# Optimization experiments

Measured on AMD Instinct MI355X. Metric: run time of the kernel, lower is better.

## Reference

```python
import jax, jax.numpy as jnp
import numpy as np

N = 100000   # nodes
E = 3200000  # edges
G = 512      # graphs in batch
EPS = 1e-5   # batchnorm eps


def _lin(key, fan_in, fan_out):
    return jax.random.normal(key, (fan_in, fan_out), jnp.float32) / np.sqrt(fan_in)


def setup_inputs() -> dict:
    key = jax.random.key(0)
    ks = jax.random.split(key, 12)
    x = jax.random.normal(ks[0], (N, 2), jnp.float32)
    edge_index = jax.random.randint(ks[1], (2, E), 0, N, dtype=jnp.int64)
    batch_index = jnp.sort(jax.random.randint(ks[2], (N,), 0, G, dtype=jnp.int64))
    w = (8, 32, 128)
    return {
        "x": x, "edge_index": edge_index, "batch_index": batch_index,
        "W1": _lin(ks[3], 2, w[0]),   "b1": jnp.zeros((w[0],), jnp.float32),
        "g1": jnp.ones((w[0],), jnp.float32),  "be1": jnp.zeros((w[0],), jnp.float32),
        "W2": _lin(ks[4], w[0], w[1]), "b2": jnp.zeros((w[1],), jnp.float32),
        "g2": jnp.ones((w[1],), jnp.float32),  "be2": jnp.zeros((w[1],), jnp.float32),
        "W3": _lin(ks[5], w[1], w[2]), "b3": jnp.zeros((w[2],), jnp.float32),
        "g3": jnp.ones((w[2],), jnp.float32),  "be3": jnp.zeros((w[2],), jnp.float32),
        "Wl": _lin(ks[6], w[2], 3),    "bl": jnp.zeros((3,), jnp.float32),
    }


def _gcn_norm(edge_index):
    # add self loops, symmetric normalization (PyG GCNConv default)
    loops = jnp.arange(N, dtype=edge_index.dtype)
    src = jnp.concatenate([edge_index[0], loops])
    dst = jnp.concatenate([edge_index[1], loops])
    deg = jax.ops.segment_sum(jnp.ones_like(dst, jnp.float32), dst, num_segments=N)
    dis = jnp.where(deg > 0, jax.lax.rsqrt(jnp.maximum(deg, 1.0)), 0.0)
    norm = dis[src] * dis[dst]  # [E+N]
    return src, dst, norm


def _gcn_conv(h, W, b, src, dst, norm):
    h = h @ W                                   # [N, out]
    msg = h[src] * norm[:, None]                # gather + scale
    return jax.ops.segment_sum(msg, dst, num_segments=N) + b


def _bn(h, g, b):
    # training-mode batchnorm over node dim
    m = jnp.mean(h, axis=0)
    v = jnp.mean(jnp.square(h - m), axis=0)
    return (h - m) * jax.lax.rsqrt(v + EPS) * g + b


def reference(x, edge_index, batch_index, W1, b1, g1, be1, W2, b2, g2, be2,
              W3, b3, g3, be3, Wl, bl):
    src, dst, norm = _gcn_norm(edge_index)
    h = _bn(jax.nn.relu(_gcn_conv(x, W1, b1, src, dst, norm)), g1, be1)
    h = _bn(jax.nn.relu(_gcn_conv(h, W2, b2, src, dst, norm)), g2, be2)
    h = _bn(jax.nn.relu(_gcn_conv(h, W3, b3, src, dst, norm)), g3, be3)
    pooled = jax.ops.segment_max(h, batch_index, num_segments=G)  # [G, 128]
    logits = pooled @ Wl + bl                                     # [G, 3]
    return jax.nn.log_softmax(logits, axis=1)
```

## Files before the change

### kernel.cpp

```cpp
#include <hip/hip_runtime.h>
#include <hip/hip_bf16.h>
#include <hip/hip_fp16.h>
#include <math.h>

#define N_NODES 100000
#define N_EDGES 3200000
#define N_GRAPHS 512
#define BN_EPS 1e-5f
#define NBIN ((N_NODES + 511) / 512)
#define CHUNK 8192
#define NCHUNK ((N_EDGES + CHUNK - 1) / CHUNK)
#define STORE_CAP (N_EDGES + 16 * NBIN * NCHUNK)
#define LSEG 98
#define NSEGB ((N_NODES + LSEG - 1) / LSEG)
#define NSTATB ((N_NODES + 127) / 128)

typedef _Float16 half8_t __attribute__((ext_vector_type(8)));
typedef float float4_t __attribute__((ext_vector_type(4)));

struct alignas(8) h4 { __half2 a, b; };
struct alignas(16) h8s { __half2 h[4]; };


__global__ void k_hist2(const int* __restrict__ dst, int* __restrict__ hists) {
    __shared__ int h[NBIN];
    for (int i = threadIdx.x; i < NBIN; i += blockDim.x) h[i] = 0;
    __syncthreads();
    int e0 = blockIdx.x * CHUNK;
    int e1 = min(e0 + CHUNK, N_EDGES);
    for (int e = e0 + threadIdx.x; e < e1; e += blockDim.x)
        atomicAdd(&h[dst[e] >> 9], 1);
    __syncthreads();
    for (int i = threadIdx.x; i < NBIN; i += blockDim.x)
        hists[i * NCHUNK + blockIdx.x] = h[i];
}

__global__ void k_scan2(int* __restrict__ hists, int* __restrict__ ghist) {
    int b = blockIdx.x;
    int lane = threadIdx.x;
    int carry = 0;
    int base = b * NCHUNK;
    for (int c0 = 0; c0 < NCHUNK; c0 += 64) {
        int c = c0 + lane;
        int v = (c < NCHUNK) ? hists[base + c] : 0;
        int pv = (v + 15) & ~15;
        int inc = pv;
#pragma unroll
        for (int off = 1; off < 64; off <<= 1) {
            int u = __shfl_up(inc, off, 64);
            if (lane >= off) inc += u;
        }
        if (c < NCHUNK) hists[base + c] = inc - pv + carry;
        carry += __shfl(inc, 63, 64);
    }
    if (lane == 0) ghist[b] = carry;
}

__global__ void k_binscan(const int* __restrict__ ghist, int* __restrict__ bbase) {
    __shared__ int sd[512];
    int t = threadIdx.x;
    int v = (t < NBIN) ? ghist[t] : 0;
    sd[t] = v;
    __syncthreads();
    for (int off = 1; off < 512; off <<= 1) {
        int u = (t >= off) ? sd[t - off] : 0;
        __syncthreads();
        sd[t] += u;
        __syncthreads();
    }
    if (t < NBIN) bbase[t] = sd[t] - v;
    if (t == 511) bbase[NBIN] = sd[511];
}

__global__ void k_scatter(const int* __restrict__ src, const int* __restrict__ dst,
                          const int* __restrict__ bbase, const int* __restrict__ hists,
                          int* __restrict__ store) {
    __shared__ int cur[NBIN];
    for (int i = threadIdx.x; i < NBIN; i += blockDim.x)
        cur[i] = bbase[i] + hists[i * NCHUNK + blockIdx.x];
    __syncthreads();
    int e0 = blockIdx.x * CHUNK;
    int e1 = min(e0 + CHUNK, N_EDGES);
    for (int e = e0 + threadIdx.x; e < e1; e += blockDim.x) {
        int d = dst[e];
        int b = d >> 9;
        int pos = atomicAdd(&cur[b], 1);
        store[pos] = (src[e] << 9) | (d & 511);
    }
    __syncthreads();
    for (int i = threadIdx.x; i < NBIN; i += blockDim.x) {
        int p = cur[i];
        int end = (p + 15) & ~15;
        for (; p < end; ++p) store[p] = -1;
    }
}

__global__ void k_csr_build(const int* __restrict__ bbase, const int* __restrict__ store,
                            const float* __restrict__ x, int* __restrict__ offs,
                            int* __restrict__ ends, float* __restrict__ dis,
                            float* __restrict__ rdis, float4* __restrict__ xd,
                            int* __restrict__ csr) {
    __shared__ int cnt[512], cur[512], wsum[4];
    int b = blockIdx.x;
    int n0 = b << 9;
    int e0 = bbase[b], e1 = bbase[b + 1];
    int t = threadIdx.x;
    int lane = t & 63, wid = t >> 6;
    if (t < 512) cnt[t] = 0;
    __syncthreads();
    for (int e = e0 + t; e < e1; e += 1024) {
        int p = store[e];
        if (p >= 0) atomicAdd(&cnt[p & 511], 1);
    }
    __syncthreads();
    int c0 = 0, c1 = 0, pair = 0, inc = 0;
    if (t < 256) {
        c0 = cnt[2 * t];
        c1 = cnt[2 * t + 1];
        pair = c0 + c1;
        inc = pair;
#pragma unroll
        for (int off = 1; off < 64; off <<= 1) {
            int u = __shfl_up(inc, off, 64);
            if (lane >= off) inc += u;
        }
        if (lane == 63) wsum[wid] = inc;
    }
    __syncthreads();
    if (t < 256) {
        int wo = 0;
        for (int w = 0; w < wid; ++w) wo += wsum[w];
        int ex = inc - pair + wo;
        cur[2 * t] = ex;
        cur[2 * t + 1] = ex + c0;
#pragma unroll
        for (int j = 0; j < 2; ++j) {
            int n = n0 + 2 * t + j;
            int cc = j ? c1 : c0;
            int exx = j ? ex + c0 : ex;
            if (n < N_NODES) {
                offs[n] = e0 + exx;
                ends[n] = e0 + exx + cc;
                float dn = rsqrtf(1.0f + (float)cc);
                dis[n] = dn;
                rdis[n] = sqrtf(1.0f + (float)cc);
                float2 xv = *(const float2*)(x + 2 * (size_t)n);
                xd[n] = make_float4(dn * xv.x, dn * xv.y, dn, 0.f);
            } else if (n == N_NODES) {
                xd[N_NODES] = make_float4(0.f, 0.f, 0.f, 0.f);
            }
        }
    }
    __syncthreads();
    for (int e = e0 + t; e < e1; e += 1024) {
        int p = store[e];
        if (p >= 0) {
            int pos = e0 + atomicAdd(&cur[p & 511], 1);
            csr[pos] = p >> 9;
        }
    }
}


__global__ void k_agg1(const float4* __restrict__ xd, const int* __restrict__ offs,
                       const int* __restrict__ ends, const int* __restrict__ csr,
                       const float* __restrict__ W1, const float* __restrict__ b1,
                       float* __restrict__ svec, __half* __restrict__ ys1) {
    __shared__ float sW[16], sb[8];
    int t = threadIdx.x;
    if (t < 16) sW[t] = W1[t];
    if (t < 8) sb[t] = b1[t];
    __syncthreads();
    int wave = t >> 6, lane = t & 63;
    int nsub = lane >> 4, eg = lane & 15;
    int node = ((blockIdx.x * 4 + wave) << 2) + nsub;
    int e0 = offs[node], e1 = ends[node];
    float ax = 0.f, ay = 0.f, as = 0.f;
    for (int e = e0 + eg; e < e1; e += 32) {
        int s0 = csr[e];
        int s1 = (e + 16 < e1) ? csr[e + 16] : N_NODES;
        float4 v0 = xd[s0];
        float4 v1 = xd[s1];
        ax += v0.x + v1.x;
        ay += v0.y + v1.y;
        as += v0.z + v1.z;
    }
#pragma unroll
    for (int off = 1; off < 16; off <<= 1) {
        ax += __shfl_xor(ax, off, 64);
        ay += __shfl_xor(ay, off, 64);
        as += __shfl_xor(as, off, 64);
    }
    if (eg == 0) {
        float4 xn = xd[node];
        float dn = xn.z;
        float u0x = dn * (ax + xn.x);
        float u0y = dn * (ay + xn.y);
        svec[node] = dn * (as + xn.z);
        float y[8];
#pragma unroll
        for (int f = 0; f < 8; ++f)
            y[f] = dn * fmaxf(u0x * sW[f] + u0y * sW[8 + f] + sb[f], 0.f);
        h8s o;
#pragma unroll
        for (int q = 0; q < 4; ++q) o.h[q] = __floats2half2_rn(y[2 * q], y[2 * q + 1]);
        *(h8s*)(ys1 + (size_t)node * 8) = o;
    }
}


__global__ void k_prep2(const float* __restrict__ stats, const float* __restrict__ gamma,
                        const float* __restrict__ beta, const float* __restrict__ W2,
                        float* __restrict__ W2p, float* __restrict__ cw2,
                        __half* __restrict__ ys1) {
    __shared__ float a1[8], c1[8];
    int t = threadIdx.x;
    if (t < 8) {
        float inv_n = 1.0f / (float)N_NODES;
        float m = stats[t] * inv_n;
        float v = stats[8 + t] * inv_n - m * m;
        float a = gamma[t] * rsqrtf(v + BN_EPS);
        a1[t] = a;
        c1[t] = beta[t] - m * a;
    }
    __syncthreads();
    W2p[t] = a1[t >> 5] * W2[t];
    if (t < 32) {
        float cb = 0.f;
#pragma unroll
        for (int i = 0; i < 8; ++i) cb += c1[i] * W2[i * 32 + t];
        cw2[t] = cb;
    }
    if (t == 128) *(int4*)(ys1 + (size_t)N_NODES * 8) = make_int4(0, 0, 0, 0);
}


__global__ void k_agg2(const __half* __restrict__ ys1, const int* __restrict__ offs,
                       const int* __restrict__ ends, const int* __restrict__ csr,
                       const float* __restrict__ dis, const float* __restrict__ svec,
                       const float* __restrict__ W2p, const float* __restrict__ cw2,
                       const float* __restrict__ b2, __half* __restrict__ ys2) {
    __shared__ float sW[256], sC[32], sB[32];
    int t = threadIdx.x;
    sW[t] = W2p[t];
    if (t < 32) { sC[t] = cw2[t]; sB[t] = b2[t]; }
    __syncthreads();
    int wave = t >> 6, lane = t & 63;
    int nsub = lane >> 3, eg = (lane >> 1) & 3, chunk = lane & 1;
    int node = ((blockIdx.x * 4 + wave) << 3) + nsub;
    int e0 = offs[node], e1 = ends[node];
    float a0 = 0.f, a1 = 0.f, a2 = 0.f, a3 = 0.f;
    const __half* hp = ys1 + chunk * 4;
    for (int e = e0 + eg; e < e1; e += 8) {
        int s0 = csr[e];
        int s1 = (e + 4 < e1) ? csr[e + 4] : N_NODES;
        h4 v0 = *(const h4*)(hp + (size_t)s0 * 8);
        h4 v1 = *(const h4*)(hp + (size_t)s1 * 8);
        a0 += __low2float(v0.a) + __low2float(v1.a);
        a1 += __high2float(v0.a) + __high2float(v1.a);
        a2 += __low2float(v0.b) + __low2float(v1.b);
        a3 += __high2float(v0.b) + __high2float(v1.b);
    }
    if (eg == 0) {
        h4 v = *(const h4*)(hp + (size_t)node * 8);
        a0 += __low2float(v.a);
        a1 += __high2float(v.a);
        a2 += __low2float(v.b);
        a3 += __high2float(v.b);
    }
#pragma unroll
    for (int off = 2; off < 8; off <<= 1) {
        a0 += __shfl_xor(a0, off, 64);
        a1 += __shfl_xor(a1, off, 64);
        a2 += __shfl_xor(a2, off, 64);
        a3 += __shfl_xor(a3, off, 64);
    }
    int lb = nsub << 3;
    float u[8];
    u[0] = __shfl(a0, lb, 64);     u[1] = __shfl(a1, lb, 64);
    u[2] = __shfl(a2, lb, 64);     u[3] = __shfl(a3, lb, 64);
    u[4] = __shfl(a0, lb + 1, 64); u[5] = __shfl(a1, lb + 1, 64);
    u[6] = __shfl(a2, lb + 1, 64); u[7] = __shfl(a3, lb + 1, 64);
    float dn = dis[node];
    float sv = svec[node];
#pragma unroll
    for (int i = 0; i < 8; ++i) u[i] *= dn;
    int c0 = (lane & 7) * 4;
    float y[4];
#pragma unroll
    for (int k = 0; k < 4; ++k) {
        int col = c0 + k;
        float conv = sB[col] + sv * sC[col];
#pragma unroll
        for (int i = 0; i < 8; ++i) conv += u[i] * sW[i * 32 + col];
        y[k] = dn * fmaxf(conv, 0.f);
    }
    h4 o;
    o.a = __floats2half2_rn(y[0], y[1]);
    o.b = __floats2half2_rn(y[2], y[3]);
    *(h4*)(ys2 + (size_t)node * 32 + c0) = o;
}


__global__ void k_prep3(const float* __restrict__ stats, const float* __restrict__ gamma,
                        const float* __restrict__ beta, const float* __restrict__ W3,
                        __half* __restrict__ wfrag, float* __restrict__ cw3,
                        __half* __restrict__ ys2) {
    __shared__ float a2[32], c2[32];
    int t = threadIdx.x;
    if (t < 32) {
        float inv_n = 1.0f / (float)N_NODES;
        float m = stats[t] * inv_n;
        float v = stats[32 + t] * inv_n - m * m;
        float a = gamma[t] * rsqrtf(v + BN_EPS);
        a2[t] = a;
        c2[t] = beta[t] - m * a;
    }
    __syncthreads();
    {
        int g = t >> 6, kq = (t >> 4) & 3, c = t & 15;
#pragma unroll
        for (int j = 0; j < 8; ++j) {
            int k = kq * 8 + j;
            wfrag[(size_t)t * 8 + j] = __float2half(a2[k] * W3[k * 128 + g * 16 + c]);
        }
    }
    if (t < 128) {
        float cb = 0.f;
#pragma unroll
        for (int k = 0; k < 32; ++k) cb += c2[k] * W3[k * 128 + t];
        cw3[t] = cb;
    }
    if (t >= 480 && t < 496)
        ((__half2*)(ys2 + (size_t)N_NODES * 32))[t - 480] =
            __half2{__float2half(0.f), __float2half(0.f)};
}


__global__ void k_agg3(const __half* __restrict__ ys2, const int* __restrict__ offs,
                       const int* __restrict__ ends, const int* __restrict__ csr,
                       const float* __restrict__ dis, __half* __restrict__ u2) {
    int wave = threadIdx.x >> 6;
    int lane = threadIdx.x & 63;
    int node = blockIdx.x * 4 + wave;
    if (node >= N_NODES) return;
    int chunk = lane & 7;
    int eg = lane >> 3;
    int e0 = offs[node], e1 = ends[node];
    float ax = 0.f, ay = 0.f, az = 0.f, aw = 0.f;
    const __half* hp = ys2 + (size_t)chunk * 4;
    for (int e = e0 + eg; e < e1; e += 32) {
        int s0 = csr[e];
        int s1 = (e + 8 < e1) ? csr[e + 8] : N_NODES;
        int s2 = (e + 16 < e1) ? csr[e + 16] : N_NODES;
        int s3 = (e + 24 < e1) ? csr[e + 24] : N_NODES;
        h4 v0 = *(const h4*)(hp + (size_t)s0 * 32);
        h4 v1 = *(const h4*)(hp + (size_t)s1 * 32);
        h4 v2 = *(const h4*)(hp + (size_t)s2 * 32);
        h4 v3 = *(const h4*)(hp + (size_t)s3 * 32);
        ax += __low2float(v0.a) + __low2float(v1.a) + __low2float(v2.a) + __low2float(v3.a);
        ay += __high2float(v0.a) + __high2float(v1.a) + __high2float(v2.a) + __high2float(v3.a);
        az += __low2float(v0.b) + __low2float(v1.b) + __low2float(v2.b) + __low2float(v3.b);
        aw += __high2float(v0.b) + __high2float(v1.b) + __high2float(v2.b) + __high2float(v3.b);
    }
    if (eg == 0) {
        h4 v = *(const h4*)(hp + (size_t)node * 32);
        ax += __low2float(v.a);
        ay += __high2float(v.a);
        az += __low2float(v.b);
        aw += __high2float(v.b);
    }
#pragma unroll
    for (int off = 8; off < 64; off <<= 1) {
        ax += __shfl_xor(ax, off, 64);
        ay += __shfl_xor(ay, off, 64);
        az += __shfl_xor(az, off, 64);
        aw += __shfl_xor(aw, off, 64);
    }
    if (lane < 8) {
        float dn = dis[node];
        h4 o;
        o.a = __floats2half2_rn(dn * ax, dn * ay);
        o.b = __floats2half2_rn(dn * az, dn * aw);
        *(h4*)(u2 + (size_t)node * 32 + chunk * 4) = o;
    }
}


__global__ void k_mm_mfma(const __half* __restrict__ u2, const __half* __restrict__ wfrag,
                          const float* __restrict__ cw3, const float* __restrict__ b3,
                          const float* __restrict__ svec, const float* __restrict__ dis,
                          __half* __restrict__ ys3) {
    int wave = threadIdx.x >> 6;
    int lane = threadIdx.x & 63;
    int n0 = (blockIdx.x * 4 + wave) * 16;
    if (n0 >= N_NODES) return;
    int m = lane & 15;
    int kq = lane >> 4;

    half8_t af = *(const half8_t*)(u2 + (size_t)(n0 + m) * 32 + kq * 8);

    float4_t accs[8];
#pragma unroll
    for (int g = 0; g < 8; ++g) {
        float4_t acc = {0.f, 0.f, 0.f, 0.f};
        half8_t bf = *(const half8_t*)(wfrag + (size_t)((g * 4 + kq) * 16 + m) * 8);
        accs[g] = __builtin_amdgcn_mfma_f32_16x16x32_f16(af, bf, acc, 0, 0, 0);
    }
    float sv[4], dn[4];
#pragma unroll
    for (int r = 0; r < 4; ++r) {
        sv[r] = svec[n0 + kq * 4 + r];
        dn[r] = dis[n0 + kq * 4 + r];
    }
#pragma unroll
    for (int g = 0; g < 8; ++g) {
        float cwf = cw3[g * 16 + m];
        float bf3 = b3[g * 16 + m];
#pragma unroll
        for (int r = 0; r < 4; ++r) {
            float y = fmaxf(accs[g][r] + sv[r] * cwf + bf3, 0.f);
            ys3[(size_t)(n0 + kq * 4 + r) * 128 + g * 16 + m] = __float2half(dn[r] * y);
        }
    }
}


template <int FOUT>
__global__ void k_stats(const __half* __restrict__ ys, const float* __restrict__ rdis,
                        float* __restrict__ stats) {
    constexpr int GP = 256 / FOUT;
    int f = threadIdx.x % FOUT, g = threadIdx.x / FOUT;
    float s = 0.f, s2 = 0.f;
    for (int n = blockIdx.x * GP + g; n < N_NODES; n += gridDim.x * GP) {
        float v = __half2float(ys[(size_t)n * FOUT + f]) * rdis[n];
        s += v;
        s2 += v * v;
    }
    __shared__ float ls[256], ls2[256];
    ls[threadIdx.x] = s;
    ls2[threadIdx.x] = s2;
    __syncthreads();
    if (g == 0) {
        for (int gg = 1; gg < GP; ++gg) {
            s += ls[gg * FOUT + f];
            s2 += ls2[gg * FOUT + f];
        }
        atomicAdd(&stats[f], s);
        atomicAdd(&stats[FOUT + f], s2);
    }
}


__global__ void k_stats128(const __half* __restrict__ ys, const float* __restrict__ rdis,
                           float* __restrict__ part) {
    int t = threadIdx.x;
    int chunk = t & 15, row = t >> 4;
    int n0 = blockIdx.x * 128;
    float s[8] = {0, 0, 0, 0, 0, 0, 0, 0};
    float s2[8] = {0, 0, 0, 0, 0, 0, 0, 0};
#pragma unroll
    for (int i = 0; i < 8; ++i) {
        int n = n0 + i * 16 + row;
        if (n < N_NODES) {
            float r = rdis[n];
            h8s v = *(const h8s*)(ys + (size_t)n * 128 + chunk * 8);
#pragma unroll
            for (int q = 0; q < 4; ++q) {
                float v0 = __low2float(v.h[q]) * r;
                float v1 = __high2float(v.h[q]) * r;
                s[2 * q] += v0;  s2[2 * q] += v0 * v0;
                s[2 * q + 1] += v1;  s2[2 * q + 1] += v1 * v1;
            }
        }
    }
#pragma unroll
    for (int off = 16; off < 64; off <<= 1)
#pragma unroll
        for (int j = 0; j < 8; ++j) {
            s[j] += __shfl_xor(s[j], off, 64);
            s2[j] += __shfl_xor(s2[j], off, 64);
        }
    __shared__ float sm[256];
    sm[t] = 0.f;
    __syncthreads();
    if ((t & 63) < 16) {
#pragma unroll
        for (int j = 0; j < 8; ++j) {
            atomicAdd(&sm[chunk * 8 + j], s[j]);
            atomicAdd(&sm[128 + chunk * 8 + j], s2[j]);
        }
    }
    __syncthreads();
    part[(size_t)blockIdx.x * 256 + t] = sm[t];
}

__global__ void k_stats_red(const float* __restrict__ part, float* __restrict__ stats) {
    int i = blockIdx.x;
    int t = threadIdx.x;
    float s = 0.f;
    for (int b = t; b < NSTATB; b += 256) s += part[(size_t)b * 256 + i];
    __shared__ float sm[256];
    sm[t] = s;
    __syncthreads();
    for (int st = 128; st > 0; st >>= 1) {
        if (t < st) sm[t] += sm[t + st];
        __syncthreads();
    }
    if (t == 0) stats[i] = sm[0];
}


__global__ void k_pool1(const __half* __restrict__ ys3, const float* __restrict__ rdis,
                        const int* __restrict__ batch, int* __restrict__ gmax,
                        int* __restrict__ gmin) {
    __shared__ int sb[LSEG];
    __shared__ float sr[LSEG];
    int n0 = blockIdx.x * LSEG;
    int n1 = min(n0 + LSEG, N_NODES);
    int L = n1 - n0;
    int f = threadIdx.x;
    for (int i = f; i < L; i += 128) { sb[i] = batch[n0 + i]; sr[i] = rdis[n0 + i]; }
    __syncthreads();
    if (L <= 0) return;
    int cg = sb[0];
    int mx = 0;
    int mn = 0x7F800000;
    for (int i = 0; i < L; ++i) {
        int g = sb[i];
        if (g != cg) {
            atomicMax(&gmax[cg * 128 + f], mx);
            atomicMin(&gmin[cg * 128 + f], mn);
            cg = g; mx = 0; mn = 0x7F800000;
        }
        float v = __half2float(ys3[(size_t)(n0 + i) * 128 + f]) * sr[i];
        int b = __float_as_int(v);
        mx = max(mx, b);
        mn = min(mn, b);
    }
    atomicMax(&gmax[cg * 128 + f], mx);
    atomicMin(&gmin[cg * 128 + f], mn);
}


__device__ __forceinline__ int lower_bound_dev(const int* __restrict__ a, int val) {
    int lo = 0, hi = N_NODES;
    while (lo < hi) {
        int mid = (lo + hi) >> 1;
        if (a[mid] < val) lo = mid + 1; else hi = mid;
    }
    return lo;
}

__global__ void k_poolhead(const int* __restrict__ gmax, const int* __restrict__ gmin,
                           const int* __restrict__ batch, const float* __restrict__ stats,
                           const float* __restrict__ gamma, const float* __restrict__ beta,
                           const float* __restrict__ Wl, const float* __restrict__ bl,
                           float* __restrict__ out) {
    int g = blockIdx.x;
    int f = threadIdx.x;
    float inv_n = 1.0f / (float)N_NODES;
    float m = stats[f] * inv_n;
    float var = stats[128 + f] * inv_n - m * m;
    float a = gamma[f] * rsqrtf(var + BN_EPS);
    float c = beta[f] - m * a;
    int s = lower_bound_dev(batch, g);
    int e = lower_bound_dev(batch, g + 1);
    float mx = __int_as_float(gmax[g * 128 + f]);
    float mn = __int_as_float(gmin[g * 128 + f]);
    float r;
    if (e > s) r = (a >= 0.f) ? (a * mx + c) : (a * mn + c);
    else r = -INFINITY;
    __shared__ float l[3][128];
    l[0][f] = r * Wl[f * 3 + 0];
    l[1][f] = r * Wl[f * 3 + 1];
    l[2][f] = r * Wl[f * 3 + 2];
    __syncthreads();
    for (int st = 64; st > 0; st >>= 1) {
        if (f < st) {
            l[0][f] += l[0][f + st];
            l[1][f] += l[1][f + st];
            l[2][f] += l[2][f + st];
        }
        __syncthreads();
    }
    if (f == 0) {
        float l0 = l[0][0] + bl[0], l1 = l[1][0] + bl[1], l2 = l[2][0] + bl[2];
        float mxl = fmaxf(l0, fmaxf(l1, l2));
        float lse = mxl + logf(expf(l0 - mxl) + expf(l1 - mxl) + expf(l2 - mxl));
        out[g * 3 + 0] = l0 - lse;
        out[g * 3 + 1] = l1 - lse;
        out[g * 3 + 2] = l2 - lse;
    }
}


extern "C" void kernel_launch(void* const* d_in, const int* in_sizes, int n_in,
                              void* d_out, int out_size, void* d_ws, size_t ws_size,
                              hipStream_t stream) {
    const float* x   = (const float*)d_in[0];
    const int* ei    = (const int*)d_in[1];
    const int* src   = ei;
    const int* dst   = ei + N_EDGES;
    const int* batch = (const int*)d_in[2];
    const float *W1 = (const float*)d_in[3],  *b1 = (const float*)d_in[4];
    const float *g1 = (const float*)d_in[5],  *be1 = (const float*)d_in[6];
    const float *W2 = (const float*)d_in[7],  *b2 = (const float*)d_in[8];
    const float *g2 = (const float*)d_in[9],  *be2 = (const float*)d_in[10];
    const float *W3 = (const float*)d_in[11], *b3 = (const float*)d_in[12];
    const float *g3 = (const float*)d_in[13], *be3 = (const float*)d_in[14];
    const float *Wl = (const float*)d_in[15], *bl = (const float*)d_in[16];
    float* out = (float*)d_out;

    int* base = (int*)d_ws;
    size_t o = 0;
    float* stats1 = (float*)(base + o); o += 256;
    float* stats2 = (float*)(base + o); o += 256;
    float* stats3 = (float*)(base + o); o += 256;
    int* gmax     = base + o; o += (size_t)N_GRAPHS * 128;
    size_t zero_words = o;
    int* gmin     = base + o; o += (size_t)N_GRAPHS * 128;
    int* bbase    = base + o; o += NBIN + 4;
    int* ghist    = base + o; o += NBIN + 4;
    int* hists    = base + o; o += ((size_t)NBIN * NCHUNK + 3) & ~3ULL;
    float* W2p    = (float*)(base + o); o += 256;
    float* cw2    = (float*)(base + o); o += 32;
    __half* wfrag = (__half*)(base + o); o += 2048;
    float* cw3    = (float*)(base + o); o += 128;
    int* offs     = base + o; o += 100000;
    int* ends     = base + o; o += 100000;
    int* store    = base + o; o += STORE_CAP;
    int* csr      = base + o; o += STORE_CAP;
    float* dis    = (float*)(base + o); o += N_NODES;
    float* rdis   = (float*)(base + o); o += N_NODES;
    float* svec   = (float*)(base + o); o += N_NODES;
    float* spart  = (float*)(base + o); o += (size_t)NSTATB * 256;
    float4* xd    = (float4*)(base + o); o += (size_t)(N_NODES + 1) * 4;
    __half* ys1   = (__half*)(base + o); o += (size_t)(N_NODES + 1) * 4;
    __half* ys2   = (__half*)(base + o); o += (size_t)(N_NODES + 1) * 16;
    __half* u2    = (__half*)(base + o); o += (size_t)N_NODES * 16;
    __half* ys3   = (__half*)(base + o); o += (size_t)N_NODES * 64;
    if (ws_size < o * 4) return;

    const int TB = 256;

    hipMemsetAsync(base, 0, zero_words * 4, stream);
    hipMemsetAsync(gmin, 0x7F, (size_t)N_GRAPHS * 128 * 4, stream);

    k_hist2<<<NCHUNK, TB, 0, stream>>>(dst, hists);
    k_scan2<<<NBIN, 64, 0, stream>>>(hists, ghist);
    k_binscan<<<1, 512, 0, stream>>>(ghist, bbase);
    k_scatter<<<NCHUNK, TB, 0, stream>>>(src, dst, bbase, hists, store);
    k_csr_build<<<NBIN, 1024, 0, stream>>>(bbase, store, x, offs, ends, dis, rdis, xd, csr);

    k_agg1<<<N_NODES / 16, TB, 0, stream>>>(xd, offs, ends, csr, W1, b1, svec, ys1);
    k_stats<8><<<256, 256, 0, stream>>>(ys1, rdis, stats1);
    k_prep2<<<1, 256, 0, stream>>>(stats1, g1, be1, W2, W2p, cw2, ys1);

    k_agg2<<<N_NODES / 32, TB, 0, stream>>>(ys1, offs, ends, csr, dis, svec, W2p, cw2, b2, ys2);
    k_stats<32><<<256, 256, 0, stream>>>(ys2, rdis, stats2);
    k_prep3<<<1, 512, 0, stream>>>(stats2, g2, be2, W3, wfrag, cw3, ys2);

    k_agg3<<<(N_NODES + 3) / 4, TB, 0, stream>>>(ys2, offs, ends, csr, dis, u2);
    k_mm_mfma<<<(N_NODES + 63) / 64, 256, 0, stream>>>(u2, wfrag, cw3, b3, svec, dis, ys3);
    k_stats128<<<NSTATB, 256, 0, stream>>>(ys3, rdis, spart);
    k_stats_red<<<256, 256, 0, stream>>>(spart, stats3);

    k_pool1<<<NSEGB, 128, 0, stream>>>(ys3, rdis, batch, gmax, gmin);
    k_poolhead<<<N_GRAPHS, 128, 0, stream>>>(gmax, gmin, batch, stats3, g3, be3, Wl, bl, out);
}
```

Baseline: 375.8 us.

## Split layer-2 features into two 16-channel planes and aggregate each plane separately

The 32-channel fp16 layer-2 output is stored as two separate planes of 16 channels each, so every node row in a plane is 32 bytes. The layer-3 aggregation now runs as two launches, one per plane, with each wave handling two nodes. This keeps each gather pass's working set to half the feature array, which is meant to improve cache hit rates for the random source gathers. The cost is reading the CSR and offsets twice, an extra launch, and smaller 32-byte gathers per edge. The stats and MFMA kernels are updated to index the planar layout.

```diff
diff --git a/kernel.cpp b/kernel.cpp
--- a/kernel.cpp
+++ b/kernel.cpp
@@ -14,6 +14,8 @@
 #define LSEG 98
 #define NSEGB ((N_NODES + LSEG - 1) / LSEG)
 #define NSTATB ((N_NODES + 127) / 128)
+#define PLANE2 ((size_t)(N_NODES + 1) * 16)
+#define PLANEU ((size_t)N_NODES * 16)
 
 typedef _Float16 half8_t __attribute__((ext_vector_type(8)));
 typedef float float4_t __attribute__((ext_vector_type(4)));
@@ -298,7 +300,7 @@
     h4 o;
     o.a = __floats2half2_rn(y[0], y[1]);
     o.b = __floats2half2_rn(y[2], y[3]);
-    *(h4*)(ys2 + (size_t)node * 32 + c0) = o;
+    *(h4*)(ys2 + (size_t)(c0 >> 4) * PLANE2 + (size_t)node * 16 + (c0 & 15)) = o;
 }
 
 
@@ -331,58 +333,60 @@
         for (int k = 0; k < 32; ++k) cb += c2[k] * W3[k * 128 + t];
         cw3[t] = cb;
     }
-    if (t >= 480 && t < 496)
-        ((__half2*)(ys2 + (size_t)N_NODES * 32))[t - 480] =
+    if (t >= 480 && t < 496) {
+        int idx = t - 480;
+        ((__half2*)(ys2 + (size_t)(idx >> 3) * PLANE2 + (size_t)N_NODES * 16))[idx & 7] =
             __half2{__float2half(0.f), __float2half(0.f)};
+    }
 }
 
 
 __global__ void k_agg3(const __half* __restrict__ ys2, const int* __restrict__ offs,
                        const int* __restrict__ ends, const int* __restrict__ csr,
-                       const float* __restrict__ dis, __half* __restrict__ u2) {
+                       const float* __restrict__ dis, __half* __restrict__ u2, int plane) {
     int wave = threadIdx.x >> 6;
     int lane = threadIdx.x & 63;
-    int node = blockIdx.x * 4 + wave;
-    if (node >= N_NODES) return;
-    int chunk = lane & 7;
-    int eg = lane >> 3;
+    int nsub = lane >> 5;
+    int eg = (lane >> 2) & 7;
+    int chunk = lane & 3;
+    int node = ((blockIdx.x * 4 + wave) << 1) + nsub;
     int e0 = offs[node], e1 = ends[node];
     float ax = 0.f, ay = 0.f, az = 0.f, aw = 0.f;
-    const __half* hp = ys2 + (size_t)chunk * 4;
+    const __half* hp = ys2 + (size_t)plane * PLANE2 + chunk * 4;
     for (int e = e0 + eg; e < e1; e += 32) {
         int s0 = csr[e];
         int s1 = (e + 8 < e1) ? csr[e + 8] : N_NODES;
         int s2 = (e + 16 < e1) ? csr[e + 16] : N_NODES;
         int s3 = (e + 24 < e1) ? csr[e + 24] : N_NODES;
-        h4 v0 = *(const h4*)(hp + (size_t)s0 * 32);
-        h4 v1 = *(const h4*)(hp + (size_t)s1 * 32);
-        h4 v2 = *(const h4*)(hp + (size_t)s2 * 32);
-        h4 v3 = *(const h4*)(hp + (size_t)s3 * 32);
+        h4 v0 = *(const h4*)(hp + (size_t)s0 * 16);
+        h4 v1 = *(const h4*)(hp + (size_t)s1 * 16);
+        h4 v2 = *(const h4*)(hp + (size_t)s2 * 16);
+        h4 v3 = *(const h4*)(hp + (size_t)s3 * 16);
         ax += __low2float(v0.a) + __low2float(v1.a) + __low2float(v2.a) + __low2float(v3.a);
         ay += __high2float(v0.a) + __high2float(v1.a) + __high2float(v2.a) + __high2float(v3.a);
         az += __low2float(v0.b) + __low2float(v1.b) + __low2float(v2.b) + __low2float(v3.b);
         aw += __high2float(v0.b) + __high2float(v1.b) + __high2float(v2.b) + __high2float(v3.b);
     }
     if (eg == 0) {
-        h4 v = *(const h4*)(hp + (size_t)node * 32);
+        h4 v = *(const h4*)(hp + (size_t)node * 16);
         ax += __low2float(v.a);
         ay += __high2float(v.a);
         az += __low2float(v.b);
         aw += __high2float(v.b);
     }
 #pragma unroll
-    for (int off = 8; off < 64; off <<= 1) {
+    for (int off = 4; off < 32; off <<= 1) {
         ax += __shfl_xor(ax, off, 64);
         ay += __shfl_xor(ay, off, 64);
         az += __shfl_xor(az, off, 64);
         aw += __shfl_xor(aw, off, 64);
     }
-    if (lane < 8) {
+    if (eg == 0) {
         float dn = dis[node];
         h4 o;
         o.a = __floats2half2_rn(dn * ax, dn * ay);
         o.b = __floats2half2_rn(dn * az, dn * aw);
-        *(h4*)(u2 + (size_t)node * 32 + chunk * 4) = o;
+        *(h4*)(u2 + (size_t)plane * PLANEU + (size_t)node * 16 + chunk * 4) = o;
     }
 }
 
@@ -398,7 +402,8 @@
     int m = lane & 15;
     int kq = lane >> 4;
 
-    half8_t af = *(const half8_t*)(u2 + (size_t)(n0 + m) * 32 + kq * 8);
+    half8_t af = *(const half8_t*)(u2 + (size_t)(kq >> 1) * PLANEU +
+                                   (size_t)(n0 + m) * 16 + (kq & 1) * 8);
 
     float4_t accs[8];
 #pragma unroll
@@ -426,14 +431,16 @@
 }
 
 
-template <int FOUT>
+template <int FOUT, bool SPLIT>
 __global__ void k_stats(const __half* __restrict__ ys, const float* __restrict__ rdis,
                         float* __restrict__ stats) {
     constexpr int GP = 256 / FOUT;
     int f = threadIdx.x % FOUT, g = threadIdx.x / FOUT;
     float s = 0.f, s2 = 0.f;
     for (int n = blockIdx.x * GP + g; n < N_NODES; n += gridDim.x * GP) {
-        float v = __half2float(ys[(size_t)n * FOUT + f]) * rdis[n];
+        size_t idx = SPLIT ? ((size_t)(f >> 4) * PLANE2 + (size_t)n * 16 + (f & 15))
+                           : ((size_t)n * FOUT + f);
+        float v = __half2float(ys[idx]) * rdis[n];
         s += v;
         s2 += v * v;
     }
@@ -654,14 +661,15 @@
     k_csr_build<<<NBIN, 1024, 0, stream>>>(bbase, store, x, offs, ends, dis, rdis, xd, csr);
 
     k_agg1<<<N_NODES / 16, TB, 0, stream>>>(xd, offs, ends, csr, W1, b1, svec, ys1);
-    k_stats<8><<<256, 256, 0, stream>>>(ys1, rdis, stats1);
+    k_stats<8, false><<<256, 256, 0, stream>>>(ys1, rdis, stats1);
     k_prep2<<<1, 256, 0, stream>>>(stats1, g1, be1, W2, W2p, cw2, ys1);
 
     k_agg2<<<N_NODES / 32, TB, 0, stream>>>(ys1, offs, ends, csr, dis, svec, W2p, cw2, b2, ys2);
-    k_stats<32><<<256, 256, 0, stream>>>(ys2, rdis, stats2);
+    k_stats<32, true><<<256, 256, 0, stream>>>(ys2, rdis, stats2);
     k_prep3<<<1, 512, 0, stream>>>(stats2, g2, be2, W3, wfrag, cw3, ys2);
 
-    k_agg3<<<(N_NODES + 3) / 4, TB, 0, stream>>>(ys2, offs, ends, csr, dis, u2);
+    k_agg3<<<N_NODES / 8, TB, 0, stream>>>(ys2, offs, ends, csr, dis, u2, 0);
+    k_agg3<<<N_NODES / 8, TB, 0, stream>>>(ys2, offs, ends, csr, dis, u2, 1);
     k_mm_mfma<<<(N_NODES + 63) / 64, 256, 0, stream>>>(u2, wfrag, cw3, b3, svec, dis, ys3);
     k_stats128<<<NSTATB, 256, 0, stream>>>(ys3, rdis, spart);
     k_stats_red<<<256, 256, 0, stream>>>(spart, stats3);
```

Result: slower. 383.3 us (+2.0%).
